# Performance work log

Hardware: AMD Instinct MI355X
Metric: run time of the kernel (lower is better)

The kernel has to match this reference:

```python
import jax, jax.numpy as jnp
import numpy as np

B, S, D, H = 2, 2048, 1024, 16
HD = D // H
SCALE = HD ** -0.5


def setup_inputs() -> dict:
    key = jax.random.key(0)
    k1, k2, k3 = jax.random.split(key, 3)
    x = jax.random.normal(k1, (B, S, D), dtype=jnp.float32)
    # causal mask: True = masked (as used by masked_fill)
    mask = jnp.triu(jnp.ones((S, S), dtype=bool), k=1)
    w_qkv = jax.random.normal(k2, (D, 3 * D), dtype=jnp.float32) * (D ** -0.5)
    b_qkv = jnp.zeros((3 * D,), dtype=jnp.float32)
    w_out = jax.random.normal(k3, (D, D), dtype=jnp.float32) * (D ** -0.5)
    b_out = jnp.zeros((D,), dtype=jnp.float32)
    return {"x": x, "mask": mask, "w_qkv": w_qkv, "b_qkv": b_qkv,
            "w_out": w_out, "b_out": b_out}


def reference(x, mask, w_qkv, b_qkv, w_out, b_out):
    # qkv projection and split
    qkv = x @ w_qkv + b_qkv                     # [b, s, 3D]
    q, k, v = jnp.split(qkv, 3, axis=-1)
    # b s (h d) -> b h s d
    def to_heads(t):
        return t.reshape(B, S, H, HD).transpose(0, 2, 1, 3)
    q, k, v = to_heads(q), to_heads(k), to_heads(v)
    # attention scores [b, h, s, s]
    scores = jnp.einsum('bhqd,bhkd->bhqk', q, k) * SCALE
    scores = jnp.where(mask, -jnp.inf, scores)
    attn = jax.nn.softmax(scores, axis=-1)      # dropout is identity (eval)
    out = jnp.einsum('bhqk,bhkd->bhqd', attn, v)
    out = out.transpose(0, 2, 1, 3).reshape(B, S, D)  # b h s d -> b s (h d)
    out = out @ w_out + b_out                   # out dropout identity (eval)
    return (out, k, v)
```

## Files before the change

kernel.cpp:

```cpp
#include <hip/hip_runtime.h>
#include <hip/hip_bf16.h>

typedef short bf16x8 __attribute__((ext_vector_type(8)));
typedef short u16x4v __attribute__((ext_vector_type(4)));
typedef float f32x4  __attribute__((ext_vector_type(4)));
typedef unsigned short u16;
typedef unsigned int   u32;

#define NB   2
#define NS   2048
#define ND   1024
#define NH   16
#define NHD  64
#define N3   3072
#define NM   4096

__device__ __forceinline__ u16 f2bf(float f) {
    u32 u;
    __builtin_memcpy(&u, &f, 4);
    u += 0x7fffu + ((u >> 16) & 1u);
    return (u16)(u >> 16);
}
__device__ __forceinline__ bf16x8 load8f(const float* f) {
    float4 a = *(const float4*)f;
    float4 b = *(const float4*)(f + 4);
    bf16x8 r;
    r[0] = (short)f2bf(a.x); r[1] = (short)f2bf(a.y);
    r[2] = (short)f2bf(a.z); r[3] = (short)f2bf(a.w);
    r[4] = (short)f2bf(b.x); r[5] = (short)f2bf(b.y);
    r[6] = (short)f2bf(b.z); r[7] = (short)f2bf(b.w);
    return r;
}
__device__ __forceinline__ void gload_lds16(const void* g, void* l) {
    __builtin_amdgcn_global_load_lds(
        (const __attribute__((address_space(1))) u32*)g,
        (__attribute__((address_space(3))) u32*)l, 16, 0, 0);
}
__device__ __forceinline__ float hexp2(float x) {
    return __builtin_amdgcn_exp2f(x);
}

__global__ __launch_bounds__(256) void prep_cvt(
    const float* __restrict__ X, u16* __restrict__ Xb,
    const float* __restrict__ Wqkv, u16* __restrict__ WqkvT,
    const float* __restrict__ Wout, u16* __restrict__ WoutT)
{
    __shared__ float t[32][33];
    const int b = blockIdx.x;
    if (b < 2048) {
        const int i = (b * 256 + threadIdx.x) * 8;
        *(bf16x8*)(Xb + i) = load8f(X + i);
        return;
    }
    const float* in; u16* outp; int R, C, tIdx;
    if (b < 5120) { in = Wqkv; outp = WqkvT; R = ND; C = N3; tIdx = b - 2048; }
    else          { in = Wout; outp = WoutT; R = ND; C = ND; tIdx = b - 5120; }
    const int nbc = C >> 5;
    const int r0 = (tIdx / nbc) << 5;
    const int c0 = (tIdx % nbc) << 5;
    const int tr = threadIdx.x >> 3, tc = (threadIdx.x & 7) << 2;
    const float4 v = *(const float4*)(in + (size_t)(r0 + tr) * C + c0 + tc);
    t[tr][tc] = v.x; t[tr][tc + 1] = v.y; t[tr][tc + 2] = v.z; t[tr][tc + 3] = v.w;
    __syncthreads();
    u16x4v ov;
    ov[0] = (short)f2bf(t[tc + 0][tr]); ov[1] = (short)f2bf(t[tc + 1][tr]);
    ov[2] = (short)f2bf(t[tc + 2][tr]); ov[3] = (short)f2bf(t[tc + 3][tr]);
    *(u16x4v*)(outp + (size_t)(c0 + tr) * R + r0 + tc) = ov;
}

template<bool BF>
__global__ __launch_bounds__(256) void qkv_gemm(
    const float* __restrict__ Xf, const u16* __restrict__ Xb,
    const float* __restrict__ Wf, const u16* __restrict__ WbT,
    const float* __restrict__ bias,
    u16* __restrict__ q_ws, u16* __restrict__ vT_ws, u16* __restrict__ k_ws,
    float* __restrict__ k_out, float* __restrict__ v_out)
{
    __shared__ __align__(16) u16 As[2][128 * 64];
    __shared__ __align__(16) u16 Bs[2][128 * 64];

    const int bm = blockIdx.x & 31;
    const int bn = blockIdx.x >> 5;
    const int m0 = bm * 128, n0 = bn * 128;
    const int tid = threadIdx.x;
    const int lane = tid & 63, wv = tid >> 6;
    const int wm = wv >> 1, wn = wv & 1;
    const int li = lane & 15, lg = lane >> 4;
    const int gsw = ((lane & 7) * 16) ^ ((lane >> 3) << 4);
    const int rsw = (li & 7) << 3;

    f32x4 acc[4][4];
    #pragma unroll
    for (int i = 0; i < 4; ++i)
        #pragma unroll
        for (int j = 0; j < 4; ++j)
            acc[i][j] = (f32x4){0.f, 0.f, 0.f, 0.f};

    auto stage = [&](int B, int k0) {
        if constexpr (BF) {
            #pragma unroll
            for (int i = 0; i < 4; ++i) {
                const int r0 = (i * 4 + wv) * 8;
                gload_lds16((const char*)(Xb  + (size_t)(m0 + r0 + (lane >> 3)) * ND + k0) + gsw, &As[B][r0 * 64]);
                gload_lds16((const char*)(WbT + (size_t)(n0 + r0 + (lane >> 3)) * ND + k0) + gsw, &Bs[B][r0 * 64]);
            }
        } else {
            #pragma unroll
            for (int i = 0; i < 4; ++i) {
                const int row = 32 * i + (tid >> 3), col = (tid & 7) * 8;
                *(bf16x8*)(&As[B][row * 64 + (col ^ ((row & 7) * 8))]) =
                    load8f(Xf + (size_t)(m0 + row) * ND + k0 + col);
            }
            #pragma unroll
            for (int i = 0; i < 4; ++i) {
                const int krow = 16 * i + (tid >> 4), ncol = (tid & 15) * 8;
                bf16x8 bv = load8f(Wf + (size_t)(k0 + krow) * N3 + n0 + ncol);
                #pragma unroll
                for (int jj = 0; jj < 8; ++jj) {
                    const int n_ = ncol + jj;
                    Bs[B][n_ * 64 + ((((krow >> 3) ^ (n_ & 7)) << 3) | (krow & 7))] = (u16)bv[jj];
                }
            }
        }
    };

    stage(0, 0);
    __syncthreads();

    int buf = 0;
    for (int k0 = 0; k0 < ND; k0 += 64) {
        if (k0 + 64 < ND) stage(buf ^ 1, k0 + 64);

        bf16x8 a[4][2], b[4][2];
        #pragma unroll
        for (int i = 0; i < 4; ++i)
            #pragma unroll
            for (int kk = 0; kk < 2; ++kk)
                a[i][kk] = *(const bf16x8*)(&As[buf][(wm * 64 + i * 16 + li) * 64 + ((kk * 32 + lg * 8) ^ rsw)]);
        #pragma unroll
        for (int j = 0; j < 4; ++j)
            #pragma unroll
            for (int kk = 0; kk < 2; ++kk)
                b[j][kk] = *(const bf16x8*)(&Bs[buf][(wn * 64 + j * 16 + li) * 64 + ((kk * 32 + lg * 8) ^ rsw)]);
        __builtin_amdgcn_s_setprio(1);
        #pragma unroll
        for (int i = 0; i < 4; ++i)
            #pragma unroll
            for (int j = 0; j < 4; ++j) {
                acc[i][j] = __builtin_amdgcn_mfma_f32_16x16x32_bf16(a[i][0], b[j][0], acc[i][j], 0, 0, 0);
                acc[i][j] = __builtin_amdgcn_mfma_f32_16x16x32_bf16(a[i][1], b[j][1], acc[i][j], 0, 0, 0);
            }
        __builtin_amdgcn_s_setprio(0);

        __syncthreads();
        buf ^= 1;
    }

    const int cls = bn >> 3;
    if (cls == 2) {
        u16* SM = &As[0][0];
        #pragma unroll
        for (int i = 0; i < 4; ++i) {
          #pragma unroll
          for (int j = 0; j < 4; ++j) {
            const int gn = n0 + wn * 64 + j * 16 + li;
            const float bval = bias[gn];
            const int c = gn & 1023, h = c >> 6, d = c & 63;
            const int n_ = wn * 64 + j * 16 + li;
            #pragma unroll
            for (int r = 0; r < 4; ++r) {
                const int gm = m0 + wm * 64 + i * 16 + lg * 4 + r;
                const int b_ = gm >> 11, sI = gm & 2047;
                const float v = acc[i][j][r] + bval;
                __builtin_nontemporal_store(v,
                    &v_out[(((size_t)(b_ * NH + h)) * NS + sI) * NHD + d]);
                const int m_ = wm * 64 + i * 16 + lg * 4 + r;
                SM[n_ * 128 + (m_ ^ ((n_ & 7) << 3))] = f2bf(v);
            }
          }
        }
        __syncthreads();
        const int nrow = tid >> 1, mh = tid & 1;
        const int cdx = (n0 - 2048) + nrow;
        const int hh = cdx >> 6, d = cdx & 63;
        const int b_ = m0 >> 11;
        const int s0 = (m0 & 2047) + mh * 64;
        u16* dst = vT_ws + (((size_t)(b_ * NH + hh)) * NHD + d) * NS + s0;
        #pragma unroll
        for (int c8 = 0; c8 < 8; ++c8) {
            const int m_ = mh * 64 + c8 * 8;
            *(bf16x8*)(dst + c8 * 8) =
                *(const bf16x8*)(&SM[nrow * 128 + (m_ ^ ((nrow & 7) << 3))]);
        }
    } else {
        #pragma unroll
        for (int i = 0; i < 4; ++i) {
          #pragma unroll
          for (int j = 0; j < 4; ++j) {
            const int gn = n0 + wn * 64 + j * 16 + li;
            const float bval = bias[gn];
            const int c = gn & 1023, h = c >> 6, d = c & 63;
            #pragma unroll
            for (int r = 0; r < 4; ++r) {
                const int gm = m0 + wm * 64 + i * 16 + lg * 4 + r;
                const int b_ = gm >> 11, sI = gm & 2047;
                const float v = acc[i][j][r] + bval;
                const size_t hidx = (((size_t)(b_ * NH + h)) * NS + sI) * NHD + d;
                if (cls == 0) {
                    q_ws[hidx] = f2bf(v * 0.18033688011112042f);
                } else {
                    __builtin_nontemporal_store(v, &k_out[hidx]);
                    k_ws[hidx] = f2bf(v);
                }
            }
          }
        }
    }
}

__global__ __launch_bounds__(256, 4) void attn_fwd(
    u16* __restrict__ q_all, const u16* __restrict__ k_all,
    const u16* __restrict__ vT)
{
    __shared__ __align__(16) u16 Ks[2][64 * 64];
    __shared__ __align__(16) u16 Vs[2][64 * 64];
    __shared__ __align__(16) u16 Pl[4][16 * 64];

    const int tid = threadIdx.x;
    const int wv = tid >> 6, lane = tid & 63;
    const int li = lane & 15, lg = lane >> 4;
    const int bid = blockIdx.x;
    const int xcd = bid & 7, j = bid >> 3;
    const int bh  = (xcd << 2) | (j >> 5);
    const int jj  = j & 31;
    const int qt  = (j & 32) ? (31 - jj) : jj;
    const int q0  = qt * 64 + wv * 16;
    const int ntiles = qt + 1;

    u16* qp = q_all + (size_t)bh * NS * NHD;
    const u16* kp = k_all + (size_t)bh * NS * NHD;
    const u16* vp = vT + (size_t)bh * NHD * NS;

    const int rl = lane >> 3;
    const int gsw = ((lane & 7) * 16) ^ (rl << 4);
    const int rs = (li & 7) << 3;

    bf16x8 aq0 = *(const bf16x8*)(qp + (size_t)(q0 + li) * NHD + lg * 8);
    bf16x8 aq1 = *(const bf16x8*)(qp + (size_t)(q0 + li) * NHD + 32 + lg * 8);

    f32x4 o[4], ls;
    ls = (f32x4){0.f, 0.f, 0.f, 0.f};
    #pragma unroll
    for (int nf = 0; nf < 4; ++nf) o[nf] = (f32x4){0.f, 0.f, 0.f, 0.f};
    float m = 5.75f;

    const short onb = (short)0x3F80;
    const bf16x8 ones = {onb, onb, onb, onb, onb, onb, onb, onb};

    #define STAGE(B, KB) do {                                                           \
        _Pragma("unroll")                                                               \
        for (int i_ = 0; i_ < 2; ++i_) {                                                \
            const int row_ = 16 * wv + 8 * i_;                                          \
            gload_lds16((const char*)(kp + (size_t)((KB) + row_ + rl) * NHD) + gsw,     \
                        &Ks[B][row_ * 64]);                                             \
            gload_lds16((const char*)(vp + (size_t)(row_ + rl) * NS + (KB)) + gsw,      \
                        &Vs[B][row_ * 64]);                                             \
        } } while (0)

    STAGE(0, 0);
    __syncthreads();

    int buf = 0;
    for (int kt = 0; kt < ntiles; ++kt) {
        const int kb = kt * 64;
        if (kt + 1 < ntiles) STAGE(buf ^ 1, kb + 64);

        const u16* K = Ks[buf];
        const u16* V = Vs[buf];

        f32x4 s[4];
        __builtin_amdgcn_s_setprio(1);
        #pragma unroll
        for (int kq = 0; kq < 4; ++kq) {
            const u16* Kr = K + (kq * 16 + li) * 64;
            const bf16x8 b0 = *(const bf16x8*)(Kr + ((lg * 8) ^ rs));
            const bf16x8 b1 = *(const bf16x8*)(Kr + ((lg * 8 + 32) ^ rs));
            f32x4 t = (f32x4){0.f, 0.f, 0.f, 0.f};
            t = __builtin_amdgcn_mfma_f32_16x16x32_bf16(aq0, b0, t, 0, 0, 0);
            s[kq] = __builtin_amdgcn_mfma_f32_16x16x32_bf16(aq1, b1, t, 0, 0, 0);
        }
        __builtin_amdgcn_s_setprio(0);

        float mx = s[0][0];
        #pragma unroll
        for (int kq = 0; kq < 4; ++kq)
            #pragma unroll
            for (int r = 0; r < 4; ++r)
                mx = fmaxf(mx, s[kq][r]);
        if (__any(mx > m)) {
            #pragma unroll
            for (int dd = 1; dd < 64; dd <<= 1)
                mx = fmaxf(mx, __shfl_xor(mx, dd, 64));
            const float corr = hexp2(m - mx);
            m = mx;
            #pragma unroll
            for (int nf = 0; nf < 4; ++nf)
                #pragma unroll
                for (int r = 0; r < 4; ++r) o[nf][r] *= corr;
            #pragma unroll
            for (int r = 0; r < 4; ++r) ls[r] *= corr;
        }

        bf16x8 vf[4][2];
        #pragma unroll
        for (int nf = 0; nf < 4; ++nf) {
            const u16* Vr = V + (nf * 16 + li) * 64;
            vf[nf][0] = *(const bf16x8*)(Vr + ((lg * 8) ^ rs));
            vf[nf][1] = *(const bf16x8*)(Vr + ((lg * 8 + 32) ^ rs));
        }

        const bool maskt = (kt == ntiles - 1);
        u16* PW = Pl[wv];
        #pragma unroll
        for (int r = 0; r < 4; ++r) {
            const int q_ = lg * 4 + r;
            const int qrow = q0 + q_;
            const int qm = q_ & 7;
            #pragma unroll
            for (int kq = 0; kq < 4; ++kq) {
                float ev = hexp2(s[kq][r] - m);
                if (maskt && (kb + kq * 16 + li > qrow)) ev = 0.f;
                PW[q_ * 64 + ((((2 * kq + (li >> 3)) ^ qm) << 3) | (li & 7))] = f2bf(ev);
            }
        }
        asm volatile("s_waitcnt lgkmcnt(0)" ::: "memory");
        const bf16x8 pa0 = *(const bf16x8*)(PW + li * 64 + ((lg ^ (li & 7)) << 3));
        const bf16x8 pa1 = *(const bf16x8*)(PW + li * 64 + (((lg + 4) ^ (li & 7)) << 3));
        __builtin_amdgcn_s_setprio(1);
        #pragma unroll
        for (int nf = 0; nf < 4; ++nf) {
            f32x4 t = __builtin_amdgcn_mfma_f32_16x16x32_bf16(pa0, vf[nf][0], o[nf], 0, 0, 0);
            o[nf] = __builtin_amdgcn_mfma_f32_16x16x32_bf16(pa1, vf[nf][1], t, 0, 0, 0);
        }
        ls = __builtin_amdgcn_mfma_f32_16x16x32_bf16(pa0, ones, ls, 0, 0, 0);
        ls = __builtin_amdgcn_mfma_f32_16x16x32_bf16(pa1, ones, ls, 0, 0, 0);
        __builtin_amdgcn_s_setprio(0);

        __syncthreads();
        buf ^= 1;
    }

    #pragma unroll
    for (int nf = 0; nf < 4; ++nf)
        #pragma unroll
        for (int r = 0; r < 4; ++r)
            qp[(size_t)(q0 + lg * 4 + r) * NHD + nf * 16 + li] = f2bf(o[nf][r] / ls[r]);
    #undef STAGE
}

template<bool BF>
__global__ __launch_bounds__(256) void out_gemm(
    const u16* __restrict__ Aq,
    const float* __restrict__ Wf, const u16* __restrict__ WbT,
    const float* __restrict__ bias, float* __restrict__ outp)
{
    __shared__ __align__(16) u16 As[2][128 * 64];
    __shared__ __align__(16) u16 Bs[2][128 * 64];

    const int bm = blockIdx.x & 31;
    const int bn = blockIdx.x >> 5;
    const int m0 = bm * 128, n0 = bn * 128;
    const int tid = threadIdx.x;
    const int lane = tid & 63, wv = tid >> 6;
    const int wm = wv >> 1, wn = wv & 1;
    const int li = lane & 15, lg = lane >> 4;
    const int gsw = ((lane & 7) * 16) ^ ((lane >> 3) << 4);
    const int rsw = (li & 7) << 3;

    f32x4 acc[4][4];
    #pragma unroll
    for (int i = 0; i < 4; ++i)
        #pragma unroll
        for (int j = 0; j < 4; ++j)
            acc[i][j] = (f32x4){0.f, 0.f, 0.f, 0.f};

    auto stage = [&](int B, int k0) {
        const int h = k0 >> 6;
        #pragma unroll
        for (int i = 0; i < 4; ++i) {
            const int r0 = (i * 4 + wv) * 8;
            const int gm = m0 + r0 + (lane >> 3);
            const int b_ = gm >> 11, sI = gm & 2047;
            gload_lds16((const char*)(Aq + (((size_t)(b_ * NH + h)) * NS + sI) * NHD) + gsw,
                        &As[B][r0 * 64]);
            if constexpr (BF)
                gload_lds16((const char*)(WbT + (size_t)(n0 + r0 + (lane >> 3)) * ND + k0) + gsw,
                            &Bs[B][r0 * 64]);
        }
        if constexpr (!BF) {
            #pragma unroll
            for (int i = 0; i < 4; ++i) {
                const int krow = 16 * i + (tid >> 4), ncol = (tid & 15) * 8;
                bf16x8 bv = load8f(Wf + (size_t)(k0 + krow) * ND + n0 + ncol);
                #pragma unroll
                for (int jj = 0; jj < 8; ++jj) {
                    const int n_ = ncol + jj;
                    Bs[B][n_ * 64 + ((((krow >> 3) ^ (n_ & 7)) << 3) | (krow & 7))] = (u16)bv[jj];
                }
            }
        }
    };

    stage(0, 0);
    __syncthreads();

    int buf = 0;
    for (int k0 = 0; k0 < ND; k0 += 64) {
        if (k0 + 64 < ND) stage(buf ^ 1, k0 + 64);

        bf16x8 a[4][2], b[4][2];
        #pragma unroll
        for (int i = 0; i < 4; ++i)
            #pragma unroll
            for (int kk = 0; kk < 2; ++kk)
                a[i][kk] = *(const bf16x8*)(&As[buf][(wm * 64 + i * 16 + li) * 64 + ((kk * 32 + lg * 8) ^ rsw)]);
        #pragma unroll
        for (int j = 0; j < 4; ++j)
            #pragma unroll
            for (int kk = 0; kk < 2; ++kk)
                b[j][kk] = *(const bf16x8*)(&Bs[buf][(wn * 64 + j * 16 + li) * 64 + ((kk * 32 + lg * 8) ^ rsw)]);
        __builtin_amdgcn_s_setprio(1);
        #pragma unroll
        for (int i = 0; i < 4; ++i)
            #pragma unroll
            for (int j = 0; j < 4; ++j) {
                acc[i][j] = __builtin_amdgcn_mfma_f32_16x16x32_bf16(a[i][0], b[j][0], acc[i][j], 0, 0, 0);
                acc[i][j] = __builtin_amdgcn_mfma_f32_16x16x32_bf16(a[i][1], b[j][1], acc[i][j], 0, 0, 0);
            }
        __builtin_amdgcn_s_setprio(0);

        __syncthreads();
        buf ^= 1;
    }

    #pragma unroll
    for (int i = 0; i < 4; ++i) {
      #pragma unroll
      for (int j = 0; j < 4; ++j) {
        const int gn = n0 + wn * 64 + j * 16 + li;
        const float bval = bias[gn];
        #pragma unroll
        for (int r = 0; r < 4; ++r) {
            const int gm = m0 + wm * 64 + i * 16 + lg * 4 + r;
            __builtin_nontemporal_store(acc[i][j][r] + bval, &outp[(size_t)gm * ND + gn]);
        }
      }
    }
}

extern "C" void kernel_launch(void* const* d_in, const int* in_sizes, int n_in,
                              void* d_out, int out_size, void* d_ws, size_t ws_size,
                              hipStream_t stream)
{
    const float* X    = (const float*)d_in[0];
    const float* Wqkv = (const float*)d_in[2];
    const float* bqkv = (const float*)d_in[3];
    const float* Wout = (const float*)d_in[4];
    const float* bout = (const float*)d_in[5];

    const size_t HE = (size_t)NB * NH * NS * NHD;

    float* out  = (float*)d_out;
    float* kout = out + HE;
    float* vout = kout + HE;

    u16* q_ws  = (u16*)d_ws;
    u16* vT_ws = q_ws + HE;
    u16* k_ws  = vT_ws + HE;

    u16* Xb     = k_ws + HE;
    u16* WqkvT  = Xb + (size_t)NM * ND;
    u16* WoutT  = WqkvT + (size_t)ND * N3;
    const bool big = ws_size >= (size_t)41943040;

    if (big) {
        prep_cvt<<<dim3(6144), dim3(256), 0, stream>>>(X, Xb, Wqkv, WqkvT, Wout, WoutT);
        qkv_gemm<true><<<dim3(32 * 24), dim3(256), 0, stream>>>(
            X, Xb, Wqkv, WqkvT, bqkv, q_ws, vT_ws, k_ws, kout, vout);
    } else {
        qkv_gemm<false><<<dim3(32 * 24), dim3(256), 0, stream>>>(
            X, Xb, Wqkv, WqkvT, bqkv, q_ws, vT_ws, k_ws, kout, vout);
    }

    attn_fwd<<<dim3(1024), dim3(256), 0, stream>>>(q_ws, k_ws, vT_ws);

    if (big) {
        out_gemm<true><<<dim3(32 * 8), dim3(256), 0, stream>>>(
            q_ws, Wout, WoutT, bout, out);
    } else {
        out_gemm<false><<<dim3(32 * 8), dim3(256), 0, stream>>>(
            q_ws, Wout, WoutT, bout, out);
    }
}
```

Measured before the change: 115.2 us.

## Halve QKV GEMM K-tile to 32 with new swizzle, use HIP bf16 conversion

Reduces the QKV projection GEMM's K step from 64 to 32. That halves its LDS footprint (32KB instead of 64KB) so more blocks can be resident per CU, and it brings a new XOR swizzle for the 32-wide rows. It also replaces the hand-written round-to-nearest-even bf16 conversion with the HIP intrinsic __float2bfloat16, which may map to a hardware convert instruction. In exchange the loop runs twice as many iterations, each with one barrier and less MFMA work, so there is less latency hiding per sync.

```diff
diff --git a/kernel.cpp b/kernel.cpp
--- a/kernel.cpp
+++ b/kernel.cpp
@@ -20,6 +20,12 @@
     __builtin_memcpy(&u, &f, 4);
     u += 0x7fffu + ((u >> 16) & 1u);
     return (u16)(u >> 16);
+}
+__device__ __forceinline__ u16 f2bfn(float f) {
+    __hip_bfloat16 h = __float2bfloat16(f);
+    u16 r;
+    __builtin_memcpy(&r, &h, 2);
+    return r;
 }
 __device__ __forceinline__ bf16x8 load8f(const float* f) {
     float4 a = *(const float4*)f;
@@ -76,8 +82,9 @@
     u16* __restrict__ q_ws, u16* __restrict__ vT_ws, u16* __restrict__ k_ws,
     float* __restrict__ k_out, float* __restrict__ v_out)
 {
-    __shared__ __align__(16) u16 As[2][128 * 64];
-    __shared__ __align__(16) u16 Bs[2][128 * 64];
+    __shared__ __align__(16) u16 SH[16384];
+    u16* const Abase = SH;
+    u16* const Bbase = SH + 8192;
 
     const int bm = blockIdx.x & 31;
     const int bn = blockIdx.x >> 5;
@@ -86,8 +93,8 @@
     const int lane = tid & 63, wv = tid >> 6;
     const int wm = wv >> 1, wn = wv & 1;
     const int li = lane & 15, lg = lane >> 4;
-    const int gsw = ((lane & 7) * 16) ^ ((lane >> 3) << 4);
-    const int rsw = (li & 7) << 3;
+    const int rowi = lane >> 2;
+    const int gsw = (((lane & 3) ^ ((lane >> 2) & 3)) << 4);
 
     f32x4 acc[4][4];
     #pragma unroll
@@ -97,28 +104,31 @@
             acc[i][j] = (f32x4){0.f, 0.f, 0.f, 0.f};
 
     auto stage = [&](int B, int k0) {
+        u16* As_ = Abase + B * 4096;
+        u16* Bs_ = Bbase + B * 4096;
         if constexpr (BF) {
             #pragma unroll
-            for (int i = 0; i < 4; ++i) {
-                const int r0 = (i * 4 + wv) * 8;
-                gload_lds16((const char*)(Xb  + (size_t)(m0 + r0 + (lane >> 3)) * ND + k0) + gsw, &As[B][r0 * 64]);
-                gload_lds16((const char*)(WbT + (size_t)(n0 + r0 + (lane >> 3)) * ND + k0) + gsw, &Bs[B][r0 * 64]);
+            for (int i = 0; i < 2; ++i) {
+                const int r0 = wv * 32 + i * 16;
+                gload_lds16((const char*)(Xb  + (size_t)(m0 + r0 + rowi) * ND + k0) + gsw, &As_[r0 * 32]);
+                gload_lds16((const char*)(WbT + (size_t)(n0 + r0 + rowi) * ND + k0) + gsw, &Bs_[r0 * 32]);
             }
         } else {
             #pragma unroll
-            for (int i = 0; i < 4; ++i) {
-                const int row = 32 * i + (tid >> 3), col = (tid & 7) * 8;
-                *(bf16x8*)(&As[B][row * 64 + (col ^ ((row & 7) * 8))]) =
-                    load8f(Xf + (size_t)(m0 + row) * ND + k0 + col);
-            }
-            #pragma unroll
-            for (int i = 0; i < 4; ++i) {
-                const int krow = 16 * i + (tid >> 4), ncol = (tid & 15) * 8;
+            for (int i = 0; i < 2; ++i) {
+                const int e = tid * 16 + i * 8;
+                const int row = e >> 5, col = e & 31;
+                bf16x8 v = load8f(Xf + (size_t)(m0 + row) * ND + k0 + col);
+                *(bf16x8*)(&As_[row * 32 + (((col >> 3) ^ (row & 3)) << 3)]) = v;
+            }
+            #pragma unroll
+            for (int i = 0; i < 2; ++i) {
+                const int krow = (tid >> 4) + 16 * i, ncol = (tid & 15) * 8;
                 bf16x8 bv = load8f(Wf + (size_t)(k0 + krow) * N3 + n0 + ncol);
                 #pragma unroll
                 for (int jj = 0; jj < 8; ++jj) {
                     const int n_ = ncol + jj;
-                    Bs[B][n_ * 64 + ((((krow >> 3) ^ (n_ & 7)) << 3) | (krow & 7))] = (u16)bv[jj];
+                    Bs_[n_ * 32 + ((((krow >> 3) ^ (n_ & 3)) << 3) | (krow & 7))] = (u16)bv[jj];
                 }
             }
         }
@@ -128,28 +138,28 @@
     __syncthreads();
 
     int buf = 0;
-    for (int k0 = 0; k0 < ND; k0 += 64) {
-        if (k0 + 64 < ND) stage(buf ^ 1, k0 + 64);
-
-        bf16x8 a[4][2], b[4][2];
+    for (int k0 = 0; k0 < ND; k0 += 32) {
+        if (k0 + 32 < ND) stage(buf ^ 1, k0 + 32);
+
+        const u16* As_ = Abase + buf * 4096;
+        const u16* Bs_ = Bbase + buf * 4096;
+        bf16x8 a[4], b[4];
+        #pragma unroll
+        for (int i = 0; i < 4; ++i) {
+            const int row = wm * 64 + i * 16 + li;
+            a[i] = *(const bf16x8*)(&As_[row * 32 + ((lg ^ (row & 3)) << 3)]);
+        }
+        #pragma unroll
+        for (int j = 0; j < 4; ++j) {
+            const int row = wn * 64 + j * 16 + li;
+            b[j] = *(const bf16x8*)(&Bs_[row * 32 + ((lg ^ (row & 3)) << 3)]);
+        }
+        __builtin_amdgcn_s_setprio(1);
         #pragma unroll
         for (int i = 0; i < 4; ++i)
             #pragma unroll
-            for (int kk = 0; kk < 2; ++kk)
-                a[i][kk] = *(const bf16x8*)(&As[buf][(wm * 64 + i * 16 + li) * 64 + ((kk * 32 + lg * 8) ^ rsw)]);
-        #pragma unroll
-        for (int j = 0; j < 4; ++j)
-            #pragma unroll
-            for (int kk = 0; kk < 2; ++kk)
-                b[j][kk] = *(const bf16x8*)(&Bs[buf][(wn * 64 + j * 16 + li) * 64 + ((kk * 32 + lg * 8) ^ rsw)]);
-        __builtin_amdgcn_s_setprio(1);
-        #pragma unroll
-        for (int i = 0; i < 4; ++i)
-            #pragma unroll
-            for (int j = 0; j < 4; ++j) {
-                acc[i][j] = __builtin_amdgcn_mfma_f32_16x16x32_bf16(a[i][0], b[j][0], acc[i][j], 0, 0, 0);
-                acc[i][j] = __builtin_amdgcn_mfma_f32_16x16x32_bf16(a[i][1], b[j][1], acc[i][j], 0, 0, 0);
-            }
+            for (int j = 0; j < 4; ++j)
+                acc[i][j] = __builtin_amdgcn_mfma_f32_16x16x32_bf16(a[i], b[j], acc[i][j], 0, 0, 0);
         __builtin_amdgcn_s_setprio(0);
 
         __syncthreads();
@@ -158,7 +168,7 @@
 
     const int cls = bn >> 3;
     if (cls == 2) {
-        u16* SM = &As[0][0];
+        u16* SM = SH;
         #pragma unroll
         for (int i = 0; i < 4; ++i) {
           #pragma unroll
@@ -175,7 +185,7 @@
                 __builtin_nontemporal_store(v,
                     &v_out[(((size_t)(b_ * NH + h)) * NS + sI) * NHD + d]);
                 const int m_ = wm * 64 + i * 16 + lg * 4 + r;
-                SM[n_ * 128 + (m_ ^ ((n_ & 7) << 3))] = f2bf(v);
+                SM[n_ * 128 + (m_ ^ ((n_ & 7) << 3))] = f2bfn(v);
             }
           }
         }
@@ -207,10 +217,10 @@
                 const float v = acc[i][j][r] + bval;
                 const size_t hidx = (((size_t)(b_ * NH + h)) * NS + sI) * NHD + d;
                 if (cls == 0) {
-                    q_ws[hidx] = f2bf(v * 0.18033688011112042f);
+                    q_ws[hidx] = f2bfn(v * 0.18033688011112042f);
                 } else {
                     __builtin_nontemporal_store(v, &k_out[hidx]);
-                    k_ws[hidx] = f2bf(v);
+                    k_ws[hidx] = f2bfn(v);
                 }
             }
           }
@@ -330,7 +340,7 @@
             for (int kq = 0; kq < 4; ++kq) {
                 float ev = hexp2(s[kq][r] - m);
                 if (maskt && (kb + kq * 16 + li > qrow)) ev = 0.f;
-                PW[q_ * 64 + ((((2 * kq + (li >> 3)) ^ qm) << 3) | (li & 7))] = f2bf(ev);
+                PW[q_ * 64 + ((((2 * kq + (li >> 3)) ^ qm) << 3) | (li & 7))] = f2bfn(ev);
             }
         }
         asm volatile("s_waitcnt lgkmcnt(0)" ::: "memory");
@@ -354,7 +364,7 @@
     for (int nf = 0; nf < 4; ++nf)
         #pragma unroll
         for (int r = 0; r < 4; ++r)
-            qp[(size_t)(q0 + lg * 4 + r) * NHD + nf * 16 + li] = f2bf(o[nf][r] / ls[r]);
+            qp[(size_t)(q0 + lg * 4 + r) * NHD + nf * 16 + li] = f2bfn(o[nf][r] / ls[r]);
     #undef STAGE
 }
 
```

Result: no change. 113.6 us (-1.4%).
